# Performance work log

Measured on AMD Instinct MI355X. Metric: run time of the kernel, lower is better.

## Reference

```python
import jax, jax.numpy as jnp
import numpy as np

N, E, H, DK, DV = 4096, 1024, 16, 64, 64


def setup_inputs() -> dict:
    key = jax.random.key(0)
    ks = jax.random.split(key, 5)
    x = jax.random.normal(ks[0], (N, E), dtype=jnp.float32)
    # xavier-uniform-like scale for weights
    def xavier(k, shape, fan_in, fan_out):
        lim = (6.0 / (fan_in + fan_out)) ** 0.5
        return jax.random.uniform(k, shape, dtype=jnp.float32, minval=-lim, maxval=lim)
    Wq = xavier(ks[1], (H, E, DK), E, DK)
    Wk = xavier(ks[2], (H, E, DK), E, DK)
    Wv = xavier(ks[3], (H, E, DV), E, DV)
    Wo = xavier(ks[4], (H * DV, E), H * DV, E)
    return {"x": x, "Wq": Wq, "Wk": Wk, "Wv": Wv, "Wo": Wo}


def reference(x, Wq, Wk, Wv, Wo):
    d_key = Wq.shape[-1]
    # per-head projections, batched over heads: [H, N, d]
    q = jnp.einsum('ne,hed->hnd', x, Wq)
    k = jnp.einsum('ne,hed->hnd', x, Wk)
    v = jnp.einsum('ne,hed->hnd', x, Wv)
    scores = jnp.einsum('hnd,hmd->hnm', q, k) / jnp.sqrt(jnp.float32(d_key))
    attn = jax.nn.softmax(scores, axis=-1)  # non-causal full attention
    out = jnp.einsum('hnm,hmd->hnd', attn, v)  # [H, N, DV]
    # concat heads along feature dim: [N, H*DV]
    concatenated = jnp.transpose(out, (1, 0, 2)).reshape(x.shape[0], -1)
    return concatenated @ Wo
```

## Files before the change

kernel.cpp:

```cpp
#include <hip/hip_runtime.h>
#include <hip/hip_bf16.h>


typedef __attribute__((ext_vector_type(8))) short s16x8;
typedef __attribute__((ext_vector_type(4))) float f32x4;
typedef __attribute__((ext_vector_type(16))) float f32x16;

#define MFMA16(A, B, C) __builtin_amdgcn_mfma_f32_16x16x32_bf16((A), (B), (C), 0, 0, 0)
#define MFMA32(A, B, C) __builtin_amdgcn_mfma_f32_32x32x16_bf16((A), (B), (C), 0, 0, 0)

union U8 { s16x8 h; unsigned u[4]; };

__device__ __forceinline__ unsigned short f2bf(float f) {
  unsigned int u = __float_as_uint(f);
  unsigned int r = (u + 0x7FFFu + ((u >> 16) & 1u)) >> 16;
  return (unsigned short)r;
}

__device__ __forceinline__ float expv(float x) {
  float r; asm("v_exp_f32 %0, %1" : "=v"(r) : "v"(x)); return r;
}

__device__ __forceinline__ unsigned cvtpk(float lo, float hi) {
  unsigned d; asm("v_cvt_pk_bf16_f32 %0, %1, %2" : "=v"(d) : "v"(lo), "v"(hi)); return d;
}

__device__ __forceinline__ void pl32swap(unsigned& a, unsigned& b) {
  asm("v_permlane32_swap_b32 %0, %1" : "+v"(a), "+v"(b));
}

__device__ __forceinline__ void gload16(const void* g, void* l) {
  __builtin_amdgcn_global_load_lds(
      (const __attribute__((address_space(1))) unsigned*)g,
      (__attribute__((address_space(3))) unsigned*)l, 16, 0, 0);
}


__global__ __launch_bounds__(256) void convert_x(const float* __restrict__ x,
                                                 unsigned short* __restrict__ xb) {
  unsigned i = blockIdx.x * 256u + threadIdx.x;
  float4 v = reinterpret_cast<const float4*>(x)[i];
  ushort4 o;
  o.x = f2bf(v.x); o.y = f2bf(v.y); o.z = f2bf(v.z); o.w = f2bf(v.w);
  reinterpret_cast<ushort4*>(xb)[i] = o;
}

__global__ __launch_bounds__(256)
void transpose_cast(const float* __restrict__ src, unsigned short* __restrict__ dst,
                    int R, int C) {
  __shared__ float t[64][65];
  const int b = blockIdx.x, rt = blockIdx.y, ct = blockIdx.z;
  const int q = threadIdx.x & 3;
  const float* S = src + ((size_t)b * R + rt * 64) * C + ct * 64;
  {
    const int r = threadIdx.x >> 2;
#pragma unroll
    for (int i = 0; i < 4; ++i) {
      float4 v = *reinterpret_cast<const float4*>(S + (size_t)r * C + (i * 4 + q) * 4);
      t[r][(i * 4 + q) * 4 + 0] = v.x;
      t[r][(i * 4 + q) * 4 + 1] = v.y;
      t[r][(i * 4 + q) * 4 + 2] = v.z;
      t[r][(i * 4 + q) * 4 + 3] = v.w;
    }
  }
  __syncthreads();
  const int c = threadIdx.x >> 2;
  unsigned short* D = dst + ((size_t)b * C + ct * 64 + c) * R + rt * 64;
#pragma unroll
  for (int i = 0; i < 2; ++i) {
    int rb = q * 16 + i * 8;
    union { ushort4 v[2]; unsigned short s[8]; } pk;
#pragma unroll
    for (int k = 0; k < 8; ++k) pk.s[k] = f2bf(t[rb + k][c]);
    *reinterpret_cast<ushort4*>(D + rb) = pk.v[0];
    *reinterpret_cast<ushort4*>(D + rb + 4) = pk.v[1];
  }
}

__global__ __launch_bounds__(512)
void qkv_gemm(const unsigned short* __restrict__ xb,
              const unsigned short* __restrict__ wqt,
              const unsigned short* __restrict__ wkt,
              const unsigned short* __restrict__ wvt,
              unsigned short* __restrict__ Q,
              unsigned short* __restrict__ K,
              unsigned short* __restrict__ Vt) {
  __shared__ char lds[16384 + 8192];
  char* At = lds;
  char* Bl = lds + 16384;

  const int tid = threadIdx.x;
  const int w = tid >> 6, lane = tid & 63;
  const int lr = lane & 15, lg = lane >> 4;
  const int h = blockIdx.y / 3, mat = blockIdx.y % 3;
  const unsigned short* Bg = (mat == 0 ? wqt : (mat == 1 ? wkt : wvt)) + h * 65536;
  const int m0 = blockIdx.x * 128;

  f32x4 acc[4] = {};

  const int arow = w * 16 + lr;
  unsigned aoff[2], boff[4][2];
#pragma unroll
  for (int ks = 0; ks < 2; ++ks)
    aoff[ks] = (unsigned)((arow * 128 + ks * 64 + lg * 16) ^ ((arow & 7) << 4));
#pragma unroll
  for (int n = 0; n < 4; ++n)
#pragma unroll
    for (int ks = 0; ks < 2; ++ks) {
      int br = n * 16 + lr;
      boff[n][ks] = (unsigned)((br * 128 + ks * 64 + lg * 16) ^ ((br & 7) << 4));
    }

  for (int kk = 0; kk < 16; ++kk) {
#pragma unroll
    for (int i = 0; i < 2; ++i) {
      int c = tid + i * 512;
      int row = c >> 3, c16 = c & 7;
      uint4 v = *reinterpret_cast<const uint4*>(xb + (m0 + row) * 1024 + kk * 64 + c16 * 8);
      *reinterpret_cast<uint4*>(At + ((row * 128 + c16 * 16) ^ ((row & 7) << 4))) = v;
    }
    {
      int row = tid >> 3, c16 = tid & 7;
      uint4 v = *reinterpret_cast<const uint4*>(Bg + row * 1024 + kk * 64 + c16 * 8);
      *reinterpret_cast<uint4*>(Bl + ((row * 128 + c16 * 16) ^ ((row & 7) << 4))) = v;
    }
    __syncthreads();
    s16x8 af0 = *reinterpret_cast<const s16x8*>(At + aoff[0]);
    s16x8 af1 = *reinterpret_cast<const s16x8*>(At + aoff[1]);
#pragma unroll
    for (int n = 0; n < 4; ++n) {
      acc[n] = MFMA16(af0, *reinterpret_cast<const s16x8*>(Bl + boff[n][0]), acc[n]);
      acc[n] = MFMA16(af1, *reinterpret_cast<const s16x8*>(Bl + boff[n][1]), acc[n]);
    }
    __syncthreads();
  }

  const float sc = (mat == 0) ? 0.18033688011112042f : 1.0f;
  unsigned short* dst = (mat == 0 ? Q : (mat == 1 ? K : Vt));
#pragma unroll
  for (int n = 0; n < 4; ++n)
#pragma unroll
    for (int r = 0; r < 4; ++r) {
      int row = m0 + w * 16 + lg * 4 + r;
      int col = n * 16 + lr;
      unsigned short val = f2bf(acc[n][r] * sc);
      if (mat < 2) dst[h * 262144 + row * 64 + col] = val;
      else         dst[h * 262144 + col * 4096 + row] = val;
    }
}

__global__ __launch_bounds__(256)
void attn_kernel(const unsigned short* __restrict__ Q,
                 const unsigned short* __restrict__ K,
                 const unsigned short* __restrict__ Vt,
                 unsigned short* __restrict__ cc) {
  __shared__ char smem[2 * 16384 + 512];
  float* rsf = reinterpret_cast<float*>(smem + 32768);

  const int tid = threadIdx.x;
  const int w = tid >> 6, lane = tid & 63;
  const int l31 = lane & 31, hi = lane >> 5;

  const int lin = blockIdx.x;
  const int cxcd = lin & 7, t = lin >> 3;
  const int h = cxcd * 2 + (t >> 5);
  const int q0 = (t & 31) * 128;

  const unsigned short* Qh = Q + h * 262144;
  const unsigned short* Kh = K + h * 262144;
  const unsigned short* Vh = Vt + h * 262144;

  s16x8 qf[4];
#pragma unroll
  for (int d = 0; d < 4; ++d)
    qf[d] = *reinterpret_cast<const s16x8*>(Qh + (size_t)(q0 + w * 32 + l31) * 64 + d * 16 + hi * 8);

  unsigned koff[8];
#pragma unroll
  for (int k2 = 0; k2 < 2; ++k2)
#pragma unroll
    for (int d = 0; d < 4; ++d) {
      int row = k2 * 32 + l31;
      int ch = (d * 2 + hi) ^ (row & 7);
      koff[k2 * 4 + d] = (unsigned)(row * 128 + ch * 16);
    }
  unsigned voff[8];
#pragma unroll
  for (int n = 0; n < 2; ++n)
#pragma unroll
    for (int ks = 0; ks < 4; ++ks) {
      int row = n * 32 + l31;
      int ch = (ks * 2 + hi) ^ (row & 7);
      voff[n * 4 + ks] = (unsigned)(row * 128 + ch * 16);
    }

  const int so = ((lane & 7) ^ (lane >> 3)) * 8;
  const int rsub = lane >> 3;
  auto stage = [&](int kt, char* buf) {
    char* bK = buf;
    char* bV = buf + 8192;
    const unsigned short* Ksrc = Kh + (size_t)kt * 4096;
    const unsigned short* Vsrc = Vh + kt * 64;
    gload16(Ksrc + (w * 16 + rsub) * 64 + so,                bK + w * 2048);
    gload16(Ksrc + (w * 16 + 8 + rsub) * 64 + so,            bK + w * 2048 + 1024);
    gload16(Vsrc + (size_t)(w * 16 + rsub) * 4096 + so,      bV + w * 2048);
    gload16(Vsrc + (size_t)(w * 16 + 8 + rsub) * 4096 + so,  bV + w * 2048 + 1024);
  };

  f32x16 o0 = {}, o1 = {};
  float rsl = 0.f;

  stage(0, smem);
  __syncthreads();

  for (int kt = 0; kt < 64; ++kt) {
    const int cur = kt & 1;
    char* cb = smem + cur * 16384;
    if (kt < 63) stage(kt + 1, smem + (cur ^ 1) * 16384);

    const char* bK = cb;
    const char* bV = cb + 8192;

    f32x16 s0 = {}, s1 = {};
#pragma unroll
    for (int d = 0; d < 4; ++d) {
      s16x8 a0 = *reinterpret_cast<const s16x8*>(bK + koff[d]);
      s16x8 a1 = *reinterpret_cast<const s16x8*>(bK + koff[4 + d]);
      s0 = MFMA32(a0, qf[d], s0);
      s1 = MFMA32(a1, qf[d], s1);
    }

    s16x8 pa[4];
    {
      float p[16];
#pragma unroll
      for (int r = 0; r < 16; ++r) { p[r] = expv(s0[r]); rsl += p[r]; }
      unsigned a0 = cvtpk(p[0], p[1]), b0 = cvtpk(p[2], p[3]);
      unsigned a1 = cvtpk(p[4], p[5]), b1 = cvtpk(p[6], p[7]);
      pl32swap(a0, a1); pl32swap(b0, b1);
      U8 f; f.u[0] = a0; f.u[1] = b0; f.u[2] = a1; f.u[3] = b1;
      pa[0] = f.h;
      a0 = cvtpk(p[8], p[9]);  b0 = cvtpk(p[10], p[11]);
      a1 = cvtpk(p[12], p[13]); b1 = cvtpk(p[14], p[15]);
      pl32swap(a0, a1); pl32swap(b0, b1);
      U8 g; g.u[0] = a0; g.u[1] = b0; g.u[2] = a1; g.u[3] = b1;
      pa[1] = g.h;
    }
    {
      float p[16];
#pragma unroll
      for (int r = 0; r < 16; ++r) { p[r] = expv(s1[r]); rsl += p[r]; }
      unsigned a0 = cvtpk(p[0], p[1]), b0 = cvtpk(p[2], p[3]);
      unsigned a1 = cvtpk(p[4], p[5]), b1 = cvtpk(p[6], p[7]);
      pl32swap(a0, a1); pl32swap(b0, b1);
      U8 f; f.u[0] = a0; f.u[1] = b0; f.u[2] = a1; f.u[3] = b1;
      pa[2] = f.h;
      a0 = cvtpk(p[8], p[9]);  b0 = cvtpk(p[10], p[11]);
      a1 = cvtpk(p[12], p[13]); b1 = cvtpk(p[14], p[15]);
      pl32swap(a0, a1); pl32swap(b0, b1);
      U8 g; g.u[0] = a0; g.u[1] = b0; g.u[2] = a1; g.u[3] = b1;
      pa[3] = g.h;
    }

#pragma unroll
    for (int ks = 0; ks < 4; ++ks) {
      s16x8 v0 = *reinterpret_cast<const s16x8*>(bV + voff[ks]);
      s16x8 v1 = *reinterpret_cast<const s16x8*>(bV + voff[4 + ks]);
      o0 = MFMA32(pa[ks], v0, o0);
      o1 = MFMA32(pa[ks], v1, o1);
    }

    __syncthreads();
  }

  float rst = rsl + __shfl_xor(rsl, 32, 64);
  float inv;
  asm("v_rcp_f32 %0, %1" : "=v"(inv) : "v"(rst));
  if (lane < 32) rsf[w * 32 + l31] = inv;
  __syncthreads();

#pragma unroll
  for (int reg = 0; reg < 16; ++reg) {
    int qr = (reg & 3) + 8 * (reg >> 2) + 4 * hi;
    float iv = rsf[w * 32 + qr];
    size_t base = (size_t)(q0 + w * 32 + qr) * 1024 + h * 64 + l31;
    cc[base]      = f2bf(o0[reg] * iv);
    cc[base + 32] = f2bf(o1[reg] * iv);
  }
}

__global__ __launch_bounds__(512)
void out_gemm(const unsigned short* __restrict__ A,
              const unsigned short* __restrict__ Bt,
              float* __restrict__ out) {
  __shared__ char lds[16384 + 8192];
  char* At = lds;
  char* Bl = lds + 16384;

  const int tid = threadIdx.x;
  const int w = tid >> 6, lane = tid & 63;
  const int lr = lane & 15, lg = lane >> 4;
  const int m0 = blockIdx.x * 128;
  const int n0 = blockIdx.y * 64;
  const unsigned short* Bg = Bt + n0 * 1024;

  f32x4 acc[4] = {};

  const int arow = w * 16 + lr;
  unsigned aoff[2], boff[4][2];
#pragma unroll
  for (int ks = 0; ks < 2; ++ks)
    aoff[ks] = (unsigned)((arow * 128 + ks * 64 + lg * 16) ^ ((arow & 7) << 4));
#pragma unroll
  for (int n = 0; n < 4; ++n)
#pragma unroll
    for (int ks = 0; ks < 2; ++ks) {
      int br = n * 16 + lr;
      boff[n][ks] = (unsigned)((br * 128 + ks * 64 + lg * 16) ^ ((br & 7) << 4));
    }

  for (int kk = 0; kk < 16; ++kk) {
#pragma unroll
    for (int i = 0; i < 2; ++i) {
      int c = tid + i * 512;
      int row = c >> 3, c16 = c & 7;
      uint4 v = *reinterpret_cast<const uint4*>(A + (m0 + row) * 1024 + kk * 64 + c16 * 8);
      *reinterpret_cast<uint4*>(At + ((row * 128 + c16 * 16) ^ ((row & 7) << 4))) = v;
    }
    {
      int row = tid >> 3, c16 = tid & 7;
      uint4 v = *reinterpret_cast<const uint4*>(Bg + row * 1024 + kk * 64 + c16 * 8);
      *reinterpret_cast<uint4*>(Bl + ((row * 128 + c16 * 16) ^ ((row & 7) << 4))) = v;
    }
    __syncthreads();
    s16x8 af0 = *reinterpret_cast<const s16x8*>(At + aoff[0]);
    s16x8 af1 = *reinterpret_cast<const s16x8*>(At + aoff[1]);
#pragma unroll
    for (int n = 0; n < 4; ++n) {
      acc[n] = MFMA16(af0, *reinterpret_cast<const s16x8*>(Bl + boff[n][0]), acc[n]);
      acc[n] = MFMA16(af1, *reinterpret_cast<const s16x8*>(Bl + boff[n][1]), acc[n]);
    }
    __syncthreads();
  }

#pragma unroll
  for (int n = 0; n < 4; ++n)
#pragma unroll
    for (int r = 0; r < 4; ++r) {
      int row = m0 + w * 16 + lg * 4 + r;
      int col = n0 + n * 16 + lr;
      out[row * 1024 + col] = acc[n][r];
    }
}


extern "C" void kernel_launch(void* const* d_in, const int* in_sizes, int n_in,
                              void* d_out, int out_size, void* d_ws, size_t ws_size,
                              hipStream_t stream) {
  const float* x  = (const float*)d_in[0];
  const float* Wq = (const float*)d_in[1];
  const float* Wk = (const float*)d_in[2];
  const float* Wv = (const float*)d_in[3];
  const float* Wo = (const float*)d_in[4];
  float* out = (float*)d_out;
  char* ws = (char*)d_ws;

  unsigned short* xb  = (unsigned short*)(ws);
  unsigned short* wqt = (unsigned short*)(ws + 8388608);
  unsigned short* wkt = (unsigned short*)(ws + 10485760);
  unsigned short* wvt = (unsigned short*)(ws + 12582912);
  unsigned short* wot = (unsigned short*)(ws + 14680064);
  unsigned short* Qb  = (unsigned short*)(ws + 16777216);
  unsigned short* Kb  = (unsigned short*)(ws + 25165824);
  unsigned short* Vtb = (unsigned short*)(ws + 33554432);
  unsigned short* cc  = (unsigned short*)(ws + 41943040);

  convert_x<<<4096, 256, 0, stream>>>(x, xb);
  transpose_cast<<<dim3(16, 16, 1), 256, 0, stream>>>(Wq, wqt, 1024, 64);
  transpose_cast<<<dim3(16, 16, 1), 256, 0, stream>>>(Wk, wkt, 1024, 64);
  transpose_cast<<<dim3(16, 16, 1), 256, 0, stream>>>(Wv, wvt, 1024, 64);
  transpose_cast<<<dim3(1, 16, 16), 256, 0, stream>>>(Wo, wot, 1024, 1024);

  qkv_gemm<<<dim3(32, 48), 512, 0, stream>>>(xb, wqt, wkt, wvt, Qb, Kb, Vtb);
  attn_kernel<<<512, 256, 0, stream>>>(Qb, Kb, Vtb, cc);
  out_gemm<<<dim3(32, 16), 512, 0, stream>>>(cc, wot, out);
}
```

Baseline: 252.0 us.

## Fuse QKV projections per head and enlarge GEMM tiles with direct-to-LDS loads

The QKV GEMM now computes Q, K and V for one head in a single block with a 128x192 tile, so the x tile is loaded once per head instead of three times. Each wave computes a 4x3 (qkv) or 4x2 (out) grid of MFMA tiles, which raises register-level reuse of A and B fragments. The out GEMM tile grows to 128x128. Both kernels switch their global-to-LDS staging to gload16, which relies on a helper defined outside the lines shown, and move the swizzle onto the global address. The cost is more LDS and registers per block and fewer blocks in the grid, so occupancy and wave count both drop.

```diff
diff --git a/kernel.cpp b/kernel.cpp
--- a/kernel.cpp
+++ b/kernel.cpp
@@ -77,7 +77,7 @@
   }
 }
 
-__global__ __launch_bounds__(512)
+__global__ __launch_bounds__(512, 4)
 void qkv_gemm(const unsigned short* __restrict__ xb,
               const unsigned short* __restrict__ wqt,
               const unsigned short* __restrict__ wkt,
@@ -85,68 +85,87 @@
               unsigned short* __restrict__ Q,
               unsigned short* __restrict__ K,
               unsigned short* __restrict__ Vt) {
-  __shared__ char lds[16384 + 8192];
+  __shared__ char lds[16384 + 24576];
   char* At = lds;
   char* Bl = lds + 16384;
 
   const int tid = threadIdx.x;
   const int w = tid >> 6, lane = tid & 63;
   const int lr = lane & 15, lg = lane >> 4;
-  const int h = blockIdx.y / 3, mat = blockIdx.y % 3;
-  const unsigned short* Bg = (mat == 0 ? wqt : (mat == 1 ? wkt : wvt)) + h * 65536;
+  const int mh = w >> 2, nq = w & 3;
+  const int h = blockIdx.y;
   const int m0 = blockIdx.x * 128;
 
-  f32x4 acc[4] = {};
-
-  const int arow = w * 16 + lr;
-  unsigned aoff[2], boff[4][2];
-#pragma unroll
-  for (int ks = 0; ks < 2; ++ks)
-    aoff[ks] = (unsigned)((arow * 128 + ks * 64 + lg * 16) ^ ((arow & 7) << 4));
-#pragma unroll
-  for (int n = 0; n < 4; ++n)
+  f32x4 acc[4][3] = {};
+
+  unsigned aoff[4][2], boff[3][2];
+#pragma unroll
+  for (int m = 0; m < 4; ++m) {
+    int row = mh * 64 + m * 16 + lr;
+#pragma unroll
+    for (int ks = 0; ks < 2; ++ks)
+      aoff[m][ks] = (unsigned)((row * 128 + ks * 64 + lg * 16) ^ ((row & 7) << 4));
+  }
+#pragma unroll
+  for (int n = 0; n < 3; ++n) {
+    int row = nq * 48 + n * 16 + lr;
+#pragma unroll
+    for (int ks = 0; ks < 2; ++ks)
+      boff[n][ks] = (unsigned)((row * 128 + ks * 64 + lg * 16) ^ ((row & 7) << 4));
+  }
+
+  for (int kk = 0; kk < 16; ++kk) {
+#pragma unroll
+    for (int i = 0; i < 5; ++i) {
+      int seg = w * 5 + i;
+      if (seg < 16) {
+        int row = seg * 8 + (lane >> 3);
+        int c = lane & 7;
+        gload16(xb + (size_t)(m0 + row) * 1024 + kk * 64 + ((c ^ (row & 7)) * 8),
+                At + seg * 1024);
+      } else {
+        int s2 = seg - 16;
+        int row = s2 * 8 + (lane >> 3);
+        int mat = row >> 6, mr = row & 63;
+        const unsigned short* Wb = (mat == 0 ? wqt : (mat == 1 ? wkt : wvt));
+        int c = lane & 7;
+        gload16(Wb + h * 65536 + mr * 1024 + kk * 64 + ((c ^ (row & 7)) * 8),
+                Bl + s2 * 1024);
+      }
+    }
+    __syncthreads();
 #pragma unroll
     for (int ks = 0; ks < 2; ++ks) {
-      int br = n * 16 + lr;
-      boff[n][ks] = (unsigned)((br * 128 + ks * 64 + lg * 16) ^ ((br & 7) << 4));
-    }
-
-  for (int kk = 0; kk < 16; ++kk) {
-#pragma unroll
-    for (int i = 0; i < 2; ++i) {
-      int c = tid + i * 512;
-      int row = c >> 3, c16 = c & 7;
-      uint4 v = *reinterpret_cast<const uint4*>(xb + (m0 + row) * 1024 + kk * 64 + c16 * 8);
-      *reinterpret_cast<uint4*>(At + ((row * 128 + c16 * 16) ^ ((row & 7) << 4))) = v;
-    }
-    {
-      int row = tid >> 3, c16 = tid & 7;
-      uint4 v = *reinterpret_cast<const uint4*>(Bg + row * 1024 + kk * 64 + c16 * 8);
-      *reinterpret_cast<uint4*>(Bl + ((row * 128 + c16 * 16) ^ ((row & 7) << 4))) = v;
+      s16x8 af[4], bf[3];
+#pragma unroll
+      for (int m = 0; m < 4; ++m) af[m] = *reinterpret_cast<const s16x8*>(At + aoff[m][ks]);
+#pragma unroll
+      for (int n = 0; n < 3; ++n) bf[n] = *reinterpret_cast<const s16x8*>(Bl + boff[n][ks]);
+#pragma unroll
+      for (int m = 0; m < 4; ++m)
+#pragma unroll
+        for (int n = 0; n < 3; ++n)
+          acc[m][n] = MFMA16(af[m], bf[n], acc[m][n]);
     }
     __syncthreads();
-    s16x8 af0 = *reinterpret_cast<const s16x8*>(At + aoff[0]);
-    s16x8 af1 = *reinterpret_cast<const s16x8*>(At + aoff[1]);
-#pragma unroll
-    for (int n = 0; n < 4; ++n) {
-      acc[n] = MFMA16(af0, *reinterpret_cast<const s16x8*>(Bl + boff[n][0]), acc[n]);
-      acc[n] = MFMA16(af1, *reinterpret_cast<const s16x8*>(Bl + boff[n][1]), acc[n]);
-    }
-    __syncthreads();
-  }
-
-  const float sc = (mat == 0) ? 0.18033688011112042f : 1.0f;
-  unsigned short* dst = (mat == 0 ? Q : (mat == 1 ? K : Vt));
-#pragma unroll
-  for (int n = 0; n < 4; ++n)
-#pragma unroll
-    for (int r = 0; r < 4; ++r) {
-      int row = m0 + w * 16 + lg * 4 + r;
-      int col = n * 16 + lr;
-      unsigned short val = f2bf(acc[n][r] * sc);
-      if (mat < 2) dst[h * 262144 + row * 64 + col] = val;
-      else         dst[h * 262144 + col * 4096 + row] = val;
-    }
+  }
+
+#pragma unroll
+  for (int n = 0; n < 3; ++n) {
+    int col = nq * 48 + n * 16 + lr;
+    int mat = col >> 6, d = col & 63;
+    const float sc = (mat == 0) ? 0.18033688011112042f : 1.0f;
+    unsigned short* dst = (mat == 0 ? Q : (mat == 1 ? K : Vt));
+#pragma unroll
+    for (int m = 0; m < 4; ++m)
+#pragma unroll
+      for (int r = 0; r < 4; ++r) {
+        int row = m0 + mh * 64 + m * 16 + lg * 4 + r;
+        unsigned short val = f2bf(acc[m][n][r] * sc);
+        if (mat < 2) dst[h * 262144 + row * 64 + d] = val;
+        else         dst[h * 262144 + d * 4096 + row] = val;
+      }
+  }
 }
 
 __global__ __launch_bounds__(256)
@@ -289,68 +308,79 @@
   }
 }
 
-__global__ __launch_bounds__(512)
+__global__ __launch_bounds__(512, 4)
 void out_gemm(const unsigned short* __restrict__ A,
               const unsigned short* __restrict__ Bt,
               float* __restrict__ out) {
-  __shared__ char lds[16384 + 8192];
+  __shared__ char lds[16384 + 16384];
   char* At = lds;
   char* Bl = lds + 16384;
 
   const int tid = threadIdx.x;
   const int w = tid >> 6, lane = tid & 63;
   const int lr = lane & 15, lg = lane >> 4;
+  const int mh = w >> 2, nq = w & 3;
   const int m0 = blockIdx.x * 128;
-  const int n0 = blockIdx.y * 64;
-  const unsigned short* Bg = Bt + n0 * 1024;
-
-  f32x4 acc[4] = {};
-
-  const int arow = w * 16 + lr;
-  unsigned aoff[2], boff[4][2];
-#pragma unroll
-  for (int ks = 0; ks < 2; ++ks)
-    aoff[ks] = (unsigned)((arow * 128 + ks * 64 + lg * 16) ^ ((arow & 7) << 4));
-#pragma unroll
-  for (int n = 0; n < 4; ++n)
+  const int n0 = blockIdx.y * 128;
+
+  f32x4 acc[4][2] = {};
+
+  unsigned aoff[4][2], boff[2][2];
+#pragma unroll
+  for (int m = 0; m < 4; ++m) {
+    int row = mh * 64 + m * 16 + lr;
+#pragma unroll
+    for (int ks = 0; ks < 2; ++ks)
+      aoff[m][ks] = (unsigned)((row * 128 + ks * 64 + lg * 16) ^ ((row & 7) << 4));
+  }
+#pragma unroll
+  for (int n = 0; n < 2; ++n) {
+    int row = nq * 32 + n * 16 + lr;
+#pragma unroll
+    for (int ks = 0; ks < 2; ++ks)
+      boff[n][ks] = (unsigned)((row * 128 + ks * 64 + lg * 16) ^ ((row & 7) << 4));
+  }
+
+  for (int kk = 0; kk < 16; ++kk) {
+#pragma unroll
+    for (int i = 0; i < 4; ++i) {
+      int seg = w * 4 + i;
+      int row = (seg & 15) * 8 + (lane >> 3);
+      int c = lane & 7;
+      if (seg < 16)
+        gload16(A + (size_t)(m0 + row) * 1024 + kk * 64 + ((c ^ (row & 7)) * 8),
+                At + seg * 1024);
+      else
+        gload16(Bt + (size_t)(n0 + row) * 1024 + kk * 64 + ((c ^ (row & 7)) * 8),
+                Bl + (seg - 16) * 1024);
+    }
+    __syncthreads();
 #pragma unroll
     for (int ks = 0; ks < 2; ++ks) {
-      int br = n * 16 + lr;
-      boff[n][ks] = (unsigned)((br * 128 + ks * 64 + lg * 16) ^ ((br & 7) << 4));
-    }
-
-  for (int kk = 0; kk < 16; ++kk) {
-#pragma unroll
-    for (int i = 0; i < 2; ++i) {
-      int c = tid + i * 512;
-      int row = c >> 3, c16 = c & 7;
-      uint4 v = *reinterpret_cast<const uint4*>(A + (m0 + row) * 1024 + kk * 64 + c16 * 8);
-      *reinterpret_cast<uint4*>(At + ((row * 128 + c16 * 16) ^ ((row & 7) << 4))) = v;
-    }
-    {
-      int row = tid >> 3, c16 = tid & 7;
-      uint4 v = *reinterpret_cast<const uint4*>(Bg + row * 1024 + kk * 64 + c16 * 8);
-      *reinterpret_cast<uint4*>(Bl + ((row * 128 + c16 * 16) ^ ((row & 7) << 4))) = v;
+      s16x8 af[4], bf[2];
+#pragma unroll
+      for (int m = 0; m < 4; ++m) af[m] = *reinterpret_cast<const s16x8*>(At + aoff[m][ks]);
+#pragma unroll
+      for (int n = 0; n < 2; ++n) bf[n] = *reinterpret_cast<const s16x8*>(Bl + boff[n][ks]);
+#pragma unroll
+      for (int m = 0; m < 4; ++m)
+#pragma unroll
+        for (int n = 0; n < 2; ++n)
+          acc[m][n] = MFMA16(af[m], bf[n], acc[m][n]);
     }
     __syncthreads();
-    s16x8 af0 = *reinterpret_cast<const s16x8*>(At + aoff[0]);
-    s16x8 af1 = *reinterpret_cast<const s16x8*>(At + aoff[1]);
-#pragma unroll
-    for (int n = 0; n < 4; ++n) {
-      acc[n] = MFMA16(af0, *reinterpret_cast<const s16x8*>(Bl + boff[n][0]), acc[n]);
-      acc[n] = MFMA16(af1, *reinterpret_cast<const s16x8*>(Bl + boff[n][1]), acc[n]);
-    }
-    __syncthreads();
-  }
-
-#pragma unroll
-  for (int n = 0; n < 4; ++n)
-#pragma unroll
-    for (int r = 0; r < 4; ++r) {
-      int row = m0 + w * 16 + lg * 4 + r;
-      int col = n0 + n * 16 + lr;
-      out[row * 1024 + col] = acc[n][r];
-    }
+  }
+
+#pragma unroll
+  for (int m = 0; m < 4; ++m)
+#pragma unroll
+    for (int n = 0; n < 2; ++n)
+#pragma unroll
+      for (int r = 0; r < 4; ++r) {
+        int row = m0 + mh * 64 + m * 16 + lg * 4 + r;
+        int col = n0 + nq * 32 + n * 16 + lr;
+        out[(size_t)row * 1024 + col] = acc[m][n][r];
+      }
 }
 
 
@@ -381,7 +411,7 @@
   transpose_cast<<<dim3(16, 16, 1), 256, 0, stream>>>(Wv, wvt, 1024, 64);
   transpose_cast<<<dim3(1, 16, 16), 256, 0, stream>>>(Wo, wot, 1024, 1024);
 
-  qkv_gemm<<<dim3(32, 48), 512, 0, stream>>>(xb, wqt, wkt, wvt, Qb, Kb, Vtb);
+  qkv_gemm<<<dim3(32, 16), 512, 0, stream>>>(xb, wqt, wkt, wvt, Qb, Kb, Vtb);
   attn_kernel<<<512, 256, 0, stream>>>(Qb, Kb, Vtb, cc);
-  out_gemm<<<dim3(32, 16), 512, 0, stream>>>(cc, wot, out);
-}
+  out_gemm<<<dim3(32, 8), 512, 0, stream>>>(cc, wot, out);
+}
```

New measurement: 231.0 us. 1.09x faster.
